# Optimization experiments

Hardware: AMD Instinct MI355X
Metric: run time of the kernel (lower is better)

Reference implementation:

```python
import jax, jax.numpy as jnp
import numpy as np

B, Q, D, H, HD, LP, M = 16, 1, 2048, 16, 128, 2048, 8192
EPS = 1e-5

def _ln(x, w, b):
    mu = jnp.mean(x, axis=-1, keepdims=True)
    var = jnp.mean((x - mu) ** 2, axis=-1, keepdims=True)
    return (x - mu) * jax.lax.rsqrt(var + EPS) * w + b

def setup_inputs() -> dict:
    key = jax.random.key(0)
    ks = jax.random.split(key, 8)
    std = 0.02
    return {
        "input": jax.random.normal(ks[0], (B, Q, D), jnp.float32),
        "past_key": jax.random.normal(ks[1], (B, LP, H, HD), jnp.float32),
        "past_value": jax.random.normal(ks[2], (B, LP, H, HD), jnp.float32),
        "ln0_w": jnp.ones((D,), jnp.float32),
        "ln0_b": jnp.zeros((D,), jnp.float32),
        "ln1_w": jnp.ones((D,), jnp.float32),
        "ln1_b": jnp.zeros((D,), jnp.float32),
        "wqkv": jax.random.normal(ks[3], (3 * D, D), jnp.float32) * std,
        "wo": jax.random.normal(ks[4], (D, D), jnp.float32) * std,
        "fc0_w": jax.random.normal(ks[5], (M, D), jnp.float32) * std,
        "fc0_b": jnp.zeros((M,), jnp.float32),
        "fc1_w": jax.random.normal(ks[6], (D, M), jnp.float32) * std,
        "fc1_b": jnp.zeros((D,), jnp.float32),
    }

def reference(input, past_key, past_value, ln0_w, ln0_b, ln1_w, ln1_b,
              wqkv, wo, fc0_w, fc0_b, fc1_w, fc1_b):
    # norm0 + fused QKV projection (no bias)
    x = _ln(input, ln0_w, ln0_b)                       # [B,Q,D]
    qkv = (x @ wqkv.T).reshape(B, Q, 3, H, HD)
    q, k, v = qkv[:, :, 0], qkv[:, :, 1], qkv[:, :, 2]  # each [B,Q,H,HD]
    # append to KV cache
    k = jnp.concatenate([past_key, k], axis=1)          # [B,LP+Q,H,HD]
    v = jnp.concatenate([past_value, v], axis=1)
    # decode attention; q_len == 1 so no causal mask is applied (matches source)
    scores = jnp.einsum('nqhd,nkhd->nhqk', q, k) / (HD ** 0.5)
    attn = jax.nn.softmax(scores.astype(jnp.float32), axis=-1).astype(scores.dtype)
    attn_out = jnp.einsum('nhql,nlhd->nqhd', attn, v).reshape(B, Q, D)
    attn_out = attn_out @ wo.T
    h = input + attn_out
    # MLP2 with exact (erf) GELU as in torch F.gelu
    y = _ln(h, ln1_w, ln1_b)
    y = jax.nn.gelu(y @ fc0_w.T + fc0_b, approximate=False) @ fc1_w.T + fc1_b
    return h + y
```

## Files before the change

kernel.cpp:

```cpp
#include <hip/hip_runtime.h>
#include <math.h>

typedef __attribute__((ext_vector_type(4))) float f32x4;
typedef __attribute__((ext_vector_type(4))) _Float16 f16x4;

#define B_  16
#define D_  2048
#define H_  16
#define HD_ 128
#define LP_ 2048
#define M_  8192
#define QKV_R (3 * D_)
#define SCALE 0.08838834764831845f
#define LOG2E 1.4426950408889634f
#define NSPLIT 64
#define KPS 32

__device__ inline float wave_sum(float v) {
  for (int m = 32; m > 0; m >>= 1) v += __shfl_xor(v, m);
  return v;
}

__global__ void ln_kernel(const float* __restrict__ x, const float* __restrict__ w,
                          const float* __restrict__ bb, float* __restrict__ o) {
  __shared__ float sred[4];
  int b = blockIdx.x, t = threadIdx.x;
  const float* xr = x + (size_t)b * D_;
  f32x4 v0 = *(const f32x4*)(xr + t * 8);
  f32x4 v1 = *(const f32x4*)(xr + t * 8 + 4);
  float s = (v0[0] + v0[1] + v0[2] + v0[3]) + (v1[0] + v1[1] + v1[2] + v1[3]);
  s = wave_sum(s);
  if ((t & 63) == 0) sred[t >> 6] = s;
  __syncthreads();
  float mu = (sred[0] + sred[1] + sred[2] + sred[3]) * (1.0f / D_);
  __syncthreads();
  float sq = 0.f;
  for (int i = 0; i < 4; i++) {
    float d0 = v0[i] - mu; sq += d0 * d0;
    float d1 = v1[i] - mu; sq += d1 * d1;
  }
  sq = wave_sum(sq);
  if ((t & 63) == 0) sred[t >> 6] = sq;
  __syncthreads();
  float var = (sred[0] + sred[1] + sred[2] + sred[3]) * (1.0f / D_);
  float rs = rsqrtf(var + 1e-5f);
  f32x4 w0 = *(const f32x4*)(w + t * 8), w1 = *(const f32x4*)(w + t * 8 + 4);
  f32x4 c0 = *(const f32x4*)(bb + t * 8), c1 = *(const f32x4*)(bb + t * 8 + 4);
  f32x4 o0, o1;
  for (int i = 0; i < 4; i++) {
    o0[i] = (v0[i] - mu) * rs * w0[i] + c0[i];
    o1[i] = (v1[i] - mu) * rs * w1[i] + c1[i];
  }
  *(f32x4*)(o + (size_t)b * D_ + t * 8) = o0;
  *(f32x4*)(o + (size_t)b * D_ + t * 8 + 4) = o1;
}

__global__ void gemv_k(const float* __restrict__ W, const float* __restrict__ X,
                       float* __restrict__ part, int R, int K, int kc) {
  int wave = threadIdx.x >> 6, lane = threadIdx.x & 63;
  int j0 = (blockIdx.x * 4 + wave) * 16;
  int k0 = blockIdx.y * kc;
  int col = lane & 15;
  int kg  = (lane >> 4) << 2;
  const float* wp = W + (size_t)(j0 + col) * K + k0 + kg;
  const float* xp = X + (size_t)col * K + k0 + kg;
  f32x4 acc = {0.f, 0.f, 0.f, 0.f};
  #pragma unroll 4
  for (int kk = 0; kk < kc; kk += 16) {
    f32x4 av = *(const f32x4*)xp; xp += 16;
    f32x4 bv = *(const f32x4*)wp; wp += 16;
    f16x4 ah, bh;
    for (int i = 0; i < 4; i++) { ah[i] = (_Float16)av[i]; bh[i] = (_Float16)bv[i]; }
    acc = __builtin_amdgcn_mfma_f32_16x16x16f16(ah, bh, acc, 0, 0, 0);
  }
  *(f32x4*)(part + ((size_t)blockIdx.y * R + j0 + col) * 16 + kg) = acc;
}

__global__ void reduce_plain(const float* __restrict__ part, float* __restrict__ out,
                             int R, int S) {
  int i = blockIdx.x * 256 + threadIdx.x;
  int j = i >> 4, b = i & 15;
  float s = 0.f;
  for (int k = 0; k < S; k++) s += part[(size_t)k * R * 16 + i];
  out[(size_t)b * R + j] = s;
}
__global__ void reduce_resid(const float* __restrict__ part, const float* __restrict__ resid,
                             float* __restrict__ out, int R, int S) {
  int i = blockIdx.x * 256 + threadIdx.x;
  int j = i >> 4, b = i & 15;
  float s = 0.f;
  for (int k = 0; k < S; k++) s += part[(size_t)k * R * 16 + i];
  out[(size_t)b * R + j] = resid[(size_t)b * R + j] + s;
}
__global__ void reduce_bias_gelu(const float* __restrict__ part, const float* __restrict__ bias,
                                 float* __restrict__ out, int R, int S) {
  int i = blockIdx.x * 256 + threadIdx.x;
  int j = i >> 4, b = i & 15;
  float s = 0.f;
  for (int k = 0; k < S; k++) s += part[(size_t)k * R * 16 + i];
  float u = s + bias[j];
  out[(size_t)b * R + j] = 0.5f * u * (1.0f + erff(u * 0.70710678118654752f));
}
__global__ void reduce_bias_resid(const float* __restrict__ part, const float* __restrict__ bias,
                                  const float* __restrict__ resid, float* __restrict__ out,
                                  int R, int S) {
  int i = blockIdx.x * 256 + threadIdx.x;
  int j = i >> 4, b = i & 15;
  float s = 0.f;
  for (int k = 0; k < S; k++) s += part[(size_t)k * R * 16 + i];
  out[(size_t)b * R + j] = resid[(size_t)b * R + j] + s + bias[j];
}

__global__ void attn_part(const float* __restrict__ qkv, const float* __restrict__ pk,
                          const float* __restrict__ pv, float* __restrict__ pml,
                          float* __restrict__ pacc) {
  int b = blockIdx.x, split = blockIdx.y;
  int t = threadIdx.x;
  int h = t >> 4;
  size_t rowbase = ((size_t)b * LP_ + (size_t)split * KPS) * D_ + t * 8;
  const float* kb = pk + rowbase;
  const float* vb = pv + rowbase;
  f32x4 q0 = *(const f32x4*)(qkv + (size_t)b * QKV_R + t * 8);
  f32x4 q1 = *(const f32x4*)(qkv + (size_t)b * QKV_R + t * 8 + 4);
  const float s2 = SCALE * LOG2E;
  for (int i = 0; i < 4; i++) { q0[i] *= s2; q1[i] *= s2; }

  f32x4 a0 = {0.f, 0.f, 0.f, 0.f}, a1 = {0.f, 0.f, 0.f, 0.f};
  float m2 = -1e30f, den = 0.f;

  for (int l0 = 0; l0 < KPS; l0 += 4) {
    f32x4 k0[4], k1[4], v0[4], v1[4];
    #pragma unroll
    for (int c = 0; c < 4; c++) {
      size_t off = (size_t)(l0 + c) * D_;
      k0[c] = *(const f32x4*)(kb + off);
      k1[c] = *(const f32x4*)(kb + off + 4);
      v0[c] = *(const f32x4*)(vb + off);
      v1[c] = *(const f32x4*)(vb + off + 4);
    }
    #pragma unroll
    for (int c = 0; c < 4; c++) {
      float s = q0[0]*k0[c][0] + q0[1]*k0[c][1] + q0[2]*k0[c][2] + q0[3]*k0[c][3]
              + q1[0]*k1[c][0] + q1[1]*k1[c][1] + q1[2]*k1[c][2] + q1[3]*k1[c][3];
      s += __shfl_xor(s, 1); s += __shfl_xor(s, 2);
      s += __shfl_xor(s, 4); s += __shfl_xor(s, 8);
      float mn = fmaxf(m2, s);
      float corr = exp2f(m2 - mn);
      float p = exp2f(s - mn);
      m2 = mn;
      den = den * corr + p;
      for (int i = 0; i < 4; i++) {
        a0[i] = a0[i] * corr + p * v0[c][i];
        a1[i] = a1[i] * corr + p * v1[c][i];
      }
    }
  }

  if ((t & 15) == 0) {
    pml[((b * NSPLIT + split) * H_ + h) * 2]     = m2;
    pml[((b * NSPLIT + split) * H_ + h) * 2 + 1] = den;
  }
  size_t oi = (((size_t)b * NSPLIT + split) * H_ + h) * HD_ + (t & 15) * 8;
  *(f32x4*)(pacc + oi) = a0;
  *(f32x4*)(pacc + oi + 4) = a1;
}

__global__ void attn_comb(const float* __restrict__ qkv, const float* __restrict__ pml,
                          const float* __restrict__ pacc, float* __restrict__ attn_out) {
  int bh = blockIdx.x, b = bh >> 4, hh = bh & 15;
  int t = threadIdx.x;
  __shared__ float sred[2];
  float qv = qkv[(size_t)b * QKV_R + hh * HD_ + t];
  float kn = qkv[(size_t)b * QKV_R + D_ + hh * HD_ + t];
  float d = qv * kn;
  d = wave_sum(d);
  if ((t & 63) == 0) sred[t >> 6] = d;
  __syncthreads();
  float s_new = (sred[0] + sred[1]) * SCALE * LOG2E;
  float vn = qkv[(size_t)b * QKV_R + 2 * D_ + hh * HD_ + t];
  float M = s_new;
  for (int s = 0; s < NSPLIT; s++)
    M = fmaxf(M, pml[((b * NSPLIT + s) * H_ + hh) * 2]);
  float en = exp2f(s_new - M);
  float L = en;
  float o = en * vn;
  for (int s = 0; s < NSPLIT; s++) {
    float ms = pml[((b * NSPLIT + s) * H_ + hh) * 2];
    float ls = pml[((b * NSPLIT + s) * H_ + hh) * 2 + 1];
    float e = exp2f(ms - M);
    L += ls * e;
    o += pacc[(((size_t)b * NSPLIT + s) * H_ + hh) * HD_ + t] * e;
  }
  attn_out[(size_t)b * D_ + hh * HD_ + t] = o / L;
}

extern "C" void kernel_launch(void* const* d_in, const int* in_sizes, int n_in,
                              void* d_out, int out_size, void* d_ws, size_t ws_size,
                              hipStream_t stream) {
  const float* input  = (const float*)d_in[0];
  const float* pk     = (const float*)d_in[1];
  const float* pv     = (const float*)d_in[2];
  const float* ln0_w  = (const float*)d_in[3];
  const float* ln0_b  = (const float*)d_in[4];
  const float* ln1_w  = (const float*)d_in[5];
  const float* ln1_b  = (const float*)d_in[6];
  const float* wqkv   = (const float*)d_in[7];
  const float* wo     = (const float*)d_in[8];
  const float* fc0_w  = (const float*)d_in[9];
  const float* fc0_b  = (const float*)d_in[10];
  const float* fc1_w  = (const float*)d_in[11];
  const float* fc1_b  = (const float*)d_in[12];
  float* out = (float*)d_out;

  char* wsb = (char*)d_ws;
  float* x_ln     = (float*)(wsb + 0);
  float* qkv      = (float*)(wsb + 131072);
  float* attn_out = (float*)(wsb + 524288);
  float* hbuf     = (float*)(wsb + 655360);
  float* y0       = (float*)(wsb + 786432);
  float* act      = (float*)(wsb + 917504);
  float* pml      = (float*)(wsb + 1441792);
  float* pacc     = (float*)(wsb + 1572864);
  float* part     = (float*)(wsb + 9961472);

  ln_kernel<<<16, 256, 0, stream>>>(input, ln0_w, ln0_b, x_ln);
  gemv_k<<<dim3(96, 8), 256, 0, stream>>>(wqkv, x_ln, part, QKV_R, D_, 256);
  reduce_plain<<<384, 256, 0, stream>>>(part, qkv, QKV_R, 8);
  attn_part<<<dim3(B_, NSPLIT), 256, 0, stream>>>(qkv, pk, pv, pml, pacc);
  attn_comb<<<256, 128, 0, stream>>>(qkv, pml, pacc, attn_out);
  gemv_k<<<dim3(32, 16), 256, 0, stream>>>(wo, attn_out, part, D_, D_, 128);
  reduce_resid<<<128, 256, 0, stream>>>(part, input, hbuf, D_, 16);
  ln_kernel<<<16, 256, 0, stream>>>(hbuf, ln1_w, ln1_b, y0);
  gemv_k<<<dim3(128, 4), 256, 0, stream>>>(fc0_w, y0, part, M_, D_, 512);
  reduce_bias_gelu<<<512, 256, 0, stream>>>(part, fc0_b, act, M_, 4);
  gemv_k<<<dim3(32, 16), 256, 0, stream>>>(fc1_w, act, part, D_, M_, 512);
  reduce_bias_resid<<<128, 256, 0, stream>>>(part, fc1_b, hbuf, out, D_, 16);
}
```

Baseline: 209.7 us.

## Split decode attention into scores, softmax, and AV passes instead of online softmax

Replaces the single-pass flash-decoding attention (online max/rescale per key) with three kernels: QK scores written to a workspace buffer, a per-head full softmax, and a plain weighted sum over V. The combine step becomes a simple sum plus the new-token term. This drops the serial exp/rescale dependency chain and the per-key correction work. In exchange it adds two extra launches and a scores round trip through memory.

```diff
diff --git a/kernel.cpp b/kernel.cpp
--- a/kernel.cpp
+++ b/kernel.cpp
@@ -12,7 +12,6 @@
 #define M_  8192
 #define QKV_R (3 * D_)
 #define SCALE 0.08838834764831845f
-#define LOG2E 1.4426950408889634f
 #define NSPLIT 64
 #define KPS 32
 
@@ -111,54 +110,107 @@
   out[(size_t)b * R + j] = resid[(size_t)b * R + j] + s + bias[j];
 }
 
-__global__ void attn_part(const float* __restrict__ qkv, const float* __restrict__ pk,
-                          const float* __restrict__ pv, float* __restrict__ pml,
-                          float* __restrict__ pacc) {
+__global__ void attn_scores(const float* __restrict__ qkv, const float* __restrict__ pk,
+                            float* __restrict__ scores) {
   int b = blockIdx.x, split = blockIdx.y;
   int t = threadIdx.x;
   int h = t >> 4;
-  size_t rowbase = ((size_t)b * LP_ + (size_t)split * KPS) * D_ + t * 8;
-  const float* kb = pk + rowbase;
-  const float* vb = pv + rowbase;
+  __shared__ float s_t[KPS][17];
   f32x4 q0 = *(const f32x4*)(qkv + (size_t)b * QKV_R + t * 8);
   f32x4 q1 = *(const f32x4*)(qkv + (size_t)b * QKV_R + t * 8 + 4);
-  const float s2 = SCALE * LOG2E;
-  for (int i = 0; i < 4; i++) { q0[i] *= s2; q1[i] *= s2; }
-
-  f32x4 a0 = {0.f, 0.f, 0.f, 0.f}, a1 = {0.f, 0.f, 0.f, 0.f};
-  float m2 = -1e30f, den = 0.f;
-
-  for (int l0 = 0; l0 < KPS; l0 += 4) {
-    f32x4 k0[4], k1[4], v0[4], v1[4];
-    #pragma unroll
-    for (int c = 0; c < 4; c++) {
+  for (int i = 0; i < 4; i++) { q0[i] *= SCALE; q1[i] *= SCALE; }
+  const float* kb = pk + ((size_t)b * LP_ + (size_t)split * KPS) * D_ + t * 8;
+  for (int l0 = 0; l0 < KPS; l0 += 8) {
+    f32x4 k0[8], k1[8];
+    #pragma unroll
+    for (int c = 0; c < 8; c++) {
       size_t off = (size_t)(l0 + c) * D_;
       k0[c] = *(const f32x4*)(kb + off);
       k1[c] = *(const f32x4*)(kb + off + 4);
-      v0[c] = *(const f32x4*)(vb + off);
-      v1[c] = *(const f32x4*)(vb + off + 4);
-    }
-    #pragma unroll
-    for (int c = 0; c < 4; c++) {
+    }
+    #pragma unroll
+    for (int c = 0; c < 8; c++) {
       float s = q0[0]*k0[c][0] + q0[1]*k0[c][1] + q0[2]*k0[c][2] + q0[3]*k0[c][3]
               + q1[0]*k1[c][0] + q1[1]*k1[c][1] + q1[2]*k1[c][2] + q1[3]*k1[c][3];
       s += __shfl_xor(s, 1); s += __shfl_xor(s, 2);
       s += __shfl_xor(s, 4); s += __shfl_xor(s, 8);
-      float mn = fmaxf(m2, s);
-      float corr = exp2f(m2 - mn);
-      float p = exp2f(s - mn);
-      m2 = mn;
-      den = den * corr + p;
-      for (int i = 0; i < 4; i++) {
-        a0[i] = a0[i] * corr + p * v0[c][i];
-        a1[i] = a1[i] * corr + p * v1[c][i];
-      }
-    }
-  }
-
-  if ((t & 15) == 0) {
-    pml[((b * NSPLIT + split) * H_ + h) * 2]     = m2;
-    pml[((b * NSPLIT + split) * H_ + h) * 2 + 1] = den;
+      if ((t & 15) == 0) s_t[l0 + c][h] = s;
+    }
+  }
+  __syncthreads();
+  if ((t & 15) < 8) {
+    int l4 = (t & 15) * 4;
+    f32x4 o;
+    for (int i = 0; i < 4; i++) o[i] = s_t[l4 + i][h];
+    *(f32x4*)(scores + (size_t)(b * H_ + h) * LP_ + (size_t)split * KPS + l4) = o;
+  }
+}
+
+__global__ void attn_soft(const float* __restrict__ qkv, float* __restrict__ scores,
+                          float* __restrict__ pml) {
+  int bh = blockIdx.x, b = bh >> 4, h = bh & 15;
+  int t = threadIdx.x;
+  __shared__ float sred[4];
+  float prod = 0.f;
+  if (t < 128) {
+    float qv = qkv[(size_t)b * QKV_R + h * HD_ + t];
+    float kn = qkv[(size_t)b * QKV_R + D_ + h * HD_ + t];
+    prod = qv * kn;
+  }
+  prod = wave_sum(prod);
+  if ((t & 63) == 0) sred[t >> 6] = prod;
+  __syncthreads();
+  float s_new = (sred[0] + sred[1] + sred[2] + sred[3]) * SCALE;
+  __syncthreads();
+  float* sp = scores + (size_t)bh * LP_;
+  f32x4 v0 = *(const f32x4*)(sp + t * 8);
+  f32x4 v1 = *(const f32x4*)(sp + t * 8 + 4);
+  float m = s_new;
+  for (int i = 0; i < 4; i++) m = fmaxf(m, fmaxf(v0[i], v1[i]));
+  for (int mm = 32; mm > 0; mm >>= 1) m = fmaxf(m, __shfl_xor(m, mm));
+  if ((t & 63) == 0) sred[t >> 6] = m;
+  __syncthreads();
+  float M = fmaxf(fmaxf(sred[0], sred[1]), fmaxf(sred[2], sred[3]));
+  __syncthreads();
+  float ls = 0.f;
+  for (int i = 0; i < 4; i++) {
+    v0[i] = __expf(v0[i] - M); ls += v0[i];
+    v1[i] = __expf(v1[i] - M); ls += v1[i];
+  }
+  ls = wave_sum(ls);
+  if ((t & 63) == 0) sred[t >> 6] = ls;
+  __syncthreads();
+  float en = __expf(s_new - M);
+  float L = sred[0] + sred[1] + sred[2] + sred[3] + en;
+  float inv = 1.0f / L;
+  for (int i = 0; i < 4; i++) { v0[i] *= inv; v1[i] *= inv; }
+  *(f32x4*)(sp + t * 8) = v0;
+  *(f32x4*)(sp + t * 8 + 4) = v1;
+  if (t == 0) pml[bh] = en * inv;
+}
+
+__global__ void attn_av(const float* __restrict__ scores, const float* __restrict__ pv,
+                        float* __restrict__ pacc) {
+  int b = blockIdx.x, split = blockIdx.y;
+  int t = threadIdx.x, h = t >> 4;
+  const float* vb = pv + ((size_t)b * LP_ + (size_t)split * KPS) * D_ + t * 8;
+  const float* pp = scores + (size_t)(b * H_ + h) * LP_ + (size_t)split * KPS;
+  f32x4 a0 = {0.f, 0.f, 0.f, 0.f}, a1 = {0.f, 0.f, 0.f, 0.f};
+  for (int l0 = 0; l0 < KPS; l0 += 8) {
+    f32x4 p0 = *(const f32x4*)(pp + l0);
+    f32x4 p1 = *(const f32x4*)(pp + l0 + 4);
+    f32x4 w0[8], w1[8];
+    #pragma unroll
+    for (int c = 0; c < 8; c++) {
+      size_t off = (size_t)(l0 + c) * D_;
+      w0[c] = *(const f32x4*)(vb + off);
+      w1[c] = *(const f32x4*)(vb + off + 4);
+    }
+    #pragma unroll
+    for (int c = 0; c < 8; c++) {
+      float p = (c < 4) ? p0[c] : p1[c - 4];
+      for (int i = 0; i < 4; i++) { a0[i] += p * w0[c][i]; a1[i] += p * w1[c][i]; }
+    }
   }
   size_t oi = (((size_t)b * NSPLIT + split) * H_ + h) * HD_ + (t & 15) * 8;
   *(f32x4*)(pacc + oi) = a0;
@@ -167,31 +219,13 @@
 
 __global__ void attn_comb(const float* __restrict__ qkv, const float* __restrict__ pml,
                           const float* __restrict__ pacc, float* __restrict__ attn_out) {
-  int bh = blockIdx.x, b = bh >> 4, hh = bh & 15;
+  int bh = blockIdx.x, b = bh >> 4, h = bh & 15;
   int t = threadIdx.x;
-  __shared__ float sred[2];
-  float qv = qkv[(size_t)b * QKV_R + hh * HD_ + t];
-  float kn = qkv[(size_t)b * QKV_R + D_ + hh * HD_ + t];
-  float d = qv * kn;
-  d = wave_sum(d);
-  if ((t & 63) == 0) sred[t >> 6] = d;
-  __syncthreads();
-  float s_new = (sred[0] + sred[1]) * SCALE * LOG2E;
-  float vn = qkv[(size_t)b * QKV_R + 2 * D_ + hh * HD_ + t];
-  float M = s_new;
+  float o = 0.f;
   for (int s = 0; s < NSPLIT; s++)
-    M = fmaxf(M, pml[((b * NSPLIT + s) * H_ + hh) * 2]);
-  float en = exp2f(s_new - M);
-  float L = en;
-  float o = en * vn;
-  for (int s = 0; s < NSPLIT; s++) {
-    float ms = pml[((b * NSPLIT + s) * H_ + hh) * 2];
-    float ls = pml[((b * NSPLIT + s) * H_ + hh) * 2 + 1];
-    float e = exp2f(ms - M);
-    L += ls * e;
-    o += pacc[(((size_t)b * NSPLIT + s) * H_ + hh) * HD_ + t] * e;
-  }
-  attn_out[(size_t)b * D_ + hh * HD_ + t] = o / L;
+    o += pacc[(((size_t)b * NSPLIT + s) * H_ + h) * HD_ + t];
+  o += pml[bh] * qkv[(size_t)b * QKV_R + 2 * D_ + h * HD_ + t];
+  attn_out[(size_t)b * D_ + h * HD_ + t] = o;
 }
 
 extern "C" void kernel_launch(void* const* d_in, const int* in_sizes, int n_in,
@@ -219,14 +253,17 @@
   float* hbuf     = (float*)(wsb + 655360);
   float* y0       = (float*)(wsb + 786432);
   float* act      = (float*)(wsb + 917504);
-  float* pml      = (float*)(wsb + 1441792);
-  float* pacc     = (float*)(wsb + 1572864);
-  float* part     = (float*)(wsb + 9961472);
+  float* scores   = (float*)(wsb + 1441792);
+  float* pml      = (float*)(wsb + 3538944);
+  float* pacc     = (float*)(wsb + 3543040);
+  float* part     = (float*)(wsb + 11931648);
 
   ln_kernel<<<16, 256, 0, stream>>>(input, ln0_w, ln0_b, x_ln);
   gemv_k<<<dim3(96, 8), 256, 0, stream>>>(wqkv, x_ln, part, QKV_R, D_, 256);
   reduce_plain<<<384, 256, 0, stream>>>(part, qkv, QKV_R, 8);
-  attn_part<<<dim3(B_, NSPLIT), 256, 0, stream>>>(qkv, pk, pv, pml, pacc);
+  attn_scores<<<dim3(B_, NSPLIT), 256, 0, stream>>>(qkv, pk, scores);
+  attn_soft<<<256, 256, 0, stream>>>(qkv, scores, pml);
+  attn_av<<<dim3(B_, NSPLIT), 256, 0, stream>>>(scores, pv, pacc);
   attn_comb<<<256, 128, 0, stream>>>(qkv, pml, pacc, attn_out);
   gemv_k<<<dim3(32, 16), 256, 0, stream>>>(wo, attn_out, part, D_, D_, 128);
   reduce_resid<<<128, 256, 0, stream>>>(part, input, hbuf, D_, 16);
```

Measured after the change: 211.1 us. No clear change (+0.7%).
